# Kernel optimization log

Hardware: AMD Instinct MI355X
Metric: run time of the kernel (lower is better)

## Reference

```python
import jax, jax.numpy as jnp
import numpy as np

B, NN, F, C, L = 64, 1024, 128, 128, 4   # graphs, nodes/graph, in_feat, hidden=out, GIN layers
N = B * NN                                # total nodes = 65536
E = 1_048_576                             # total edges (avg degree 16)
SLOPE = 0.01

def leaky(x):
    return jnp.where(x >= 0, x, SLOPE * x)

def setup_inputs() -> dict:
    key = jax.random.key(0)
    ks = jax.random.split(key, 12)
    s = 0.05
    return {
        "x": jax.random.normal(ks[0], (N, F), jnp.float32),
        "W1": jax.random.normal(ks[1], (L, F, C), jnp.float32) * s,
        "b1": jnp.zeros((L, C), jnp.float32),
        "W2": jax.random.normal(ks[2], (L, C, C), jnp.float32) * s,
        "b2": jnp.zeros((L, C), jnp.float32),
        "fc1_w": jax.random.normal(ks[3], (1, C), jnp.float32) * s,
        "fc1_b": jnp.zeros((1,), jnp.float32),
        "fc2_w": jax.random.normal(ks[4], (2, NN), jnp.float32) * s,
        "fc2_b": jnp.zeros((2,), jnp.float32),
        "edge_index": jax.random.randint(ks[5], (2, E), 0, N, dtype=jnp.int64),
        "batch": jax.random.randint(ks[6], (N,), 0, B, dtype=jnp.int64),
    }

def reference(x, W1, b1, W2, b2, fc1_w, fc1_b, fc2_w, fc2_b, edge_index, batch):
    src, dst = edge_index[0], edge_index[1]
    h = x
    for l in range(L):
        # GINConv: (1+eps)*x + sum_{j->i} x_j, eps=0; then MLP Lin->LeakyReLU->Lin
        agg = jax.ops.segment_sum(h[src], dst, num_segments=N)   # [N, C]
        h = h + agg
        h = leaky(h @ W1[l] + b1[l]) @ W2[l] + b2[l]
        if l < L - 1:                                            # BasicGNN act after all but last conv
            h = leaky(h)
    h = h.reshape(B, NN, C)
    y = (leaky(h) @ fc1_w.T + fc1_b).reshape(B, NN)              # FC1: C -> 1
    logits = leaky(y) @ fc2_w.T + fc2_b                         # FC2: NN -> 2
    return jax.nn.log_softmax(logits, axis=1)
```

## Files before the change

### kernel.cpp

```cpp
#include <hip/hip_runtime.h>
#include <hip/hip_bf16.h>

#define NTOT   65536
#define CDIM   128
#define NE     1048576
#define NGRAPH 64
#define NNODE  1024
#define NLAYER 4
#define SLOPE  0.01f
#define PAD    64

typedef __attribute__((ext_vector_type(8))) short short8;
typedef __attribute__((ext_vector_type(4))) float f32x4;
typedef __attribute__((ext_vector_type(8))) unsigned short ushort8v;
typedef unsigned int u32;
typedef unsigned short u16;

__device__ __forceinline__ float bf2f_lo(u32 v){ return __uint_as_float(v << 16); }
__device__ __forceinline__ float bf2f_hi(u32 v){ return __uint_as_float(v & 0xffff0000u); }
__device__ __forceinline__ u16 f2bf(float f){
    u32 u = __float_as_uint(f);
    u += 0x7fffu + ((u >> 16) & 1u);
    return (u16)(u >> 16);
}
__device__ __forceinline__ float lk(float x){ return x >= 0.f ? x : SLOPE * x; }

__device__ __forceinline__ void accm(float* a, uint4 w, bool pr){
    float f = pr ? 1.f : 0.f;
    a[0] = fmaf(f, bf2f_lo(w.x), a[0]); a[1] = fmaf(f, bf2f_hi(w.x), a[1]);
    a[2] = fmaf(f, bf2f_lo(w.y), a[2]); a[3] = fmaf(f, bf2f_hi(w.y), a[3]);
    a[4] = fmaf(f, bf2f_lo(w.z), a[4]); a[5] = fmaf(f, bf2f_hi(w.z), a[5]);
    a[6] = fmaf(f, bf2f_lo(w.w), a[6]); a[7] = fmaf(f, bf2f_hi(w.w), a[7]);
}

__global__ void k_cast_x(const float* __restrict__ x, u16* __restrict__ h){
    int i = blockIdx.x * 256 + threadIdx.x;
    const float4* x4 = (const float4*)x;
    float4 a = x4[i * 2], b = x4[i * 2 + 1];
    u32 r0 = (u32)f2bf(a.x) | ((u32)f2bf(a.y) << 16);
    u32 r1 = (u32)f2bf(a.z) | ((u32)f2bf(a.w) << 16);
    u32 r2 = (u32)f2bf(b.x) | ((u32)f2bf(b.y) << 16);
    u32 r3 = (u32)f2bf(b.z) | ((u32)f2bf(b.w) << 16);
    ((uint4*)h)[i] = make_uint4(r0, r1, r2, r3);
}

__global__ void k_conv_w(const float* __restrict__ W1, const float* __restrict__ W2,
                         u16* __restrict__ Wt){
    int idx = blockIdx.x * 256 + threadIdx.x;
    int k = idx & 127;
    int c = (idx >> 7) & 127;
    int g = (idx >> 14) & 1;
    int l = idx >> 15;
    const float* W = g ? W2 : W1;
    Wt[idx] = f2bf(W[(l * 128 + k) * 128 + c]);
}

__global__ void k_fillx(const int* __restrict__ src, const int* __restrict__ dst,
                        int* __restrict__ cnt, u16* __restrict__ csrp){
    int part = blockIdx.x & 7;
    int g    = blockIdx.x >> 3;
    int e0   = g * 2048 + threadIdx.x * 8;
    int4 d0 = *(const int4*)(dst + e0);
    int4 d1 = *(const int4*)(dst + e0 + 4);
    int4 s0 = *(const int4*)(src + e0);
    int4 s1 = *(const int4*)(src + e0 + 4);
    int d, s, p;
    #define DO_EDGE(dd, ss) d = (dd); s = (ss); \
        if ((d >> 13) == part){ p = atomicAdd(&cnt[d], 1); if (p < PAD) csrp[d * PAD + p] = (u16)s; }
    DO_EDGE(d0.x, s0.x); DO_EDGE(d0.y, s0.y); DO_EDGE(d0.z, s0.z); DO_EDGE(d0.w, s0.w);
    DO_EDGE(d1.x, s1.x); DO_EDGE(d1.y, s1.y); DO_EDGE(d1.z, s1.z); DO_EDGE(d1.w, s1.w);
    #undef DO_EDGE
}

#define LD8(P, I) \
    P##0 = h4[(size_t)(I)[0] * 16 + l16c]; \
    P##1 = h4[(size_t)(I)[1] * 16 + l16c]; \
    P##2 = h4[(size_t)(I)[2] * 16 + l16c]; \
    P##3 = h4[(size_t)(I)[3] * 16 + l16c]; \
    P##4 = h4[(size_t)(I)[4] * 16 + l16c]; \
    P##5 = h4[(size_t)(I)[5] * 16 + l16c]; \
    P##6 = h4[(size_t)(I)[6] * 16 + l16c]; \
    P##7 = h4[(size_t)(I)[7] * 16 + l16c];

#define ACC8P(P, base) \
    accm(a0, P##0, (base) + 0 < e); accm(a1, P##1, (base) + 1 < e); \
    accm(a0, P##2, (base) + 2 < e); accm(a1, P##3, (base) + 3 < e); \
    accm(a0, P##4, (base) + 4 < e); accm(a1, P##5, (base) + 5 < e); \
    accm(a0, P##6, (base) + 6 < e); accm(a1, P##7, (base) + 7 < e);

__global__ __launch_bounds__(256) void k_layer16(const u16* __restrict__ h,
                                                 const int* __restrict__ cnt,
                                                 const u16* __restrict__ csrp,
                                                 const u16* __restrict__ Wt,
                                                 const float* __restrict__ b1,
                                                 const float* __restrict__ b2,
                                                 u16* __restrict__ hout,
                                                 const float* __restrict__ fc1_w,
                                                 const float* __restrict__ fc1_b,
                                                 float* __restrict__ y,
                                                 int layer, int act, int fuse_fc1){
    __shared__ __align__(16) u16 t_lds[16][136];
    __shared__ __align__(16) u16 u_lds[16][136];
    __shared__ float fcp[4][16];
    int tid = threadIdx.x;
    int nb  = blockIdx.x;

    {
        int row  = tid >> 4;
        int l16c = tid & 15;
        int n = nb * 16 + row;
        const uint4* h4 = (const uint4*)h;
        int e = min(cnt[n], PAD);
        const u16* rowp = csrp + (size_t)n * PAD;
        int nch = (e + 7) >> 3;

        float a0[8], a1[8];
        uint4 v = h4[(size_t)n * 16 + l16c];
        a0[0] = bf2f_lo(v.x); a0[1] = bf2f_hi(v.x);
        a0[2] = bf2f_lo(v.y); a0[3] = bf2f_hi(v.y);
        a0[4] = bf2f_lo(v.z); a0[5] = bf2f_hi(v.z);
        a0[6] = bf2f_lo(v.w); a0[7] = bf2f_hi(v.w);
        for (int f = 0; f < 8; ++f) a1[f] = 0.f;

        uint4 A0, A1, A2, A3, A4, A5, A6, A7;
        uint4 B0, B1, B2, B3, B4, B5, B6, B7;
        ushort8v zer = (ushort8v)0;

        ushort8v iA = *(const ushort8v*)(rowp);
        if (nch < 1) iA = zer;
        LD8(A, iA);
        ushort8v iB = *(const ushort8v*)(rowp + 8);

        int c = 0;
        while (c < nch){
            ushort8v iu = (c + 1 < nch) ? iB : zer;
            LD8(B, iu);
            iA = *(const ushort8v*)(rowp + (size_t)(c + 2) * 8);
            ACC8P(A, c * 8);
            ++c;
            if (c >= nch) break;
            ushort8v iv = (c + 1 < nch) ? iA : zer;
            LD8(A, iv);
            iB = *(const ushort8v*)(rowp + (size_t)(c + 2) * 8);
            ACC8P(B, c * 8);
            ++c;
        }

        u32 r0 = (u32)f2bf(a0[0] + a1[0]) | ((u32)f2bf(a0[1] + a1[1]) << 16);
        u32 r1 = (u32)f2bf(a0[2] + a1[2]) | ((u32)f2bf(a0[3] + a1[3]) << 16);
        u32 r2 = (u32)f2bf(a0[4] + a1[4]) | ((u32)f2bf(a0[5] + a1[5]) << 16);
        u32 r3 = (u32)f2bf(a0[6] + a1[6]) | ((u32)f2bf(a0[7] + a1[7]) << 16);
        *(uint4*)(&t_lds[row][l16c * 8]) = make_uint4(r0, r1, r2, r3);
    }
    __syncthreads();

    int wid = tid >> 6, lane = tid & 63;
    int l16 = lane & 15, kg = lane >> 4;
    const u16* Wt1 = Wt + (size_t)(layer * 2) * 16384;
    const u16* Wt2 = Wt1 + 16384;

    f32x4 acc[2];
    acc[0] = (f32x4){0.f, 0.f, 0.f, 0.f};
    acc[1] = (f32x4){0.f, 0.f, 0.f, 0.f};
    for (int ks = 0; ks < 4; ++ks){
        int k0 = ks * 32 + kg * 8;
        short8 afrag = *(const short8*)(&t_lds[l16][k0]);
        for (int f = 0; f < 2; ++f){
            short8 bfrag = *(const short8*)(Wt1 + (size_t)(wid * 32 + f * 16 + l16) * 128 + k0);
            acc[f] = __builtin_amdgcn_mfma_f32_16x16x32_bf16(afrag, bfrag, acc[f], 0, 0, 0);
        }
    }
    for (int f = 0; f < 2; ++f){
        int col = wid * 32 + f * 16 + l16;
        float bv = b1[layer * 128 + col];
        for (int j = 0; j < 4; ++j)
            u_lds[kg * 4 + j][col] = f2bf(lk(acc[f][j] + bv));
    }
    __syncthreads();

    f32x4 acc2[2];
    acc2[0] = (f32x4){0.f, 0.f, 0.f, 0.f};
    acc2[1] = (f32x4){0.f, 0.f, 0.f, 0.f};
    for (int ks = 0; ks < 4; ++ks){
        int k0 = ks * 32 + kg * 8;
        short8 afrag = *(const short8*)(&u_lds[l16][k0]);
        for (int f = 0; f < 2; ++f){
            short8 bfrag = *(const short8*)(Wt2 + (size_t)(wid * 32 + f * 16 + l16) * 128 + k0);
            acc2[f] = __builtin_amdgcn_mfma_f32_16x16x32_bf16(afrag, bfrag, acc2[f], 0, 0, 0);
        }
    }

    if (fuse_fc1){
        float part[4] = {0.f, 0.f, 0.f, 0.f};
        for (int f = 0; f < 2; ++f){
            int col = wid * 32 + f * 16 + l16;
            float bv = b2[layer * 128 + col];
            float wv = fc1_w[col];
            for (int j = 0; j < 4; ++j)
                part[j] += lk(acc2[f][j] + bv) * wv;
        }
        for (int off = 8; off; off >>= 1)
            for (int j = 0; j < 4; ++j)
                part[j] += __shfl_xor(part[j], off, 64);
        if (l16 == 0)
            for (int j = 0; j < 4; ++j)
                fcp[wid][kg * 4 + j] = part[j];
        __syncthreads();
        if (tid < 16)
            y[nb * 16 + tid] = fcp[0][tid] + fcp[1][tid] + fcp[2][tid] + fcp[3][tid] + fc1_b[0];
    } else {
        for (int f = 0; f < 2; ++f){
            int col = wid * 32 + f * 16 + l16;
            float bv = b2[layer * 128 + col];
            for (int j = 0; j < 4; ++j){
                float v = acc2[f][j] + bv;
                if (act) v = lk(v);
                hout[(size_t)(nb * 16 + kg * 4 + j) * 128 + col] = f2bf(v);
            }
        }
    }
}

__global__ void k_fc2(const float* __restrict__ y, const float* __restrict__ fc2_w,
                      const float* __restrict__ fc2_b, float* __restrict__ out){
    int b = blockIdx.x, tid = threadIdx.x;
    float a0 = 0.f, a1 = 0.f;
    for (int j = tid; j < 1024; j += 256){
        float v = lk(y[b * 1024 + j]);
        a0 += v * fc2_w[j];
        a1 += v * fc2_w[1024 + j];
    }
    for (int off = 32; off; off >>= 1){
        a0 += __shfl_xor(a0, off, 64);
        a1 += __shfl_xor(a1, off, 64);
    }
    __shared__ float s0[4], s1[4];
    int wid = tid >> 6, lane = tid & 63;
    if (lane == 0){ s0[wid] = a0; s1[wid] = a1; }
    __syncthreads();
    if (tid == 0){
        float l0 = s0[0] + s0[1] + s0[2] + s0[3] + fc2_b[0];
        float l1 = s1[0] + s1[1] + s1[2] + s1[3] + fc2_b[1];
        float m = fmaxf(l0, l1);
        float lse = m + logf(expf(l0 - m) + expf(l1 - m));
        out[b * 2 + 0] = l0 - lse;
        out[b * 2 + 1] = l1 - lse;
    }
}

extern "C" void kernel_launch(void* const* d_in, const int* in_sizes, int n_in,
                              void* d_out, int out_size, void* d_ws, size_t ws_size,
                              hipStream_t stream){
    (void)in_sizes; (void)n_in; (void)out_size; (void)ws_size;
    const float* x     = (const float*)d_in[0];
    const float* W1    = (const float*)d_in[1];
    const float* b1    = (const float*)d_in[2];
    const float* W2    = (const float*)d_in[3];
    const float* b2    = (const float*)d_in[4];
    const float* fc1_w = (const float*)d_in[5];
    const float* fc1_b = (const float*)d_in[6];
    const float* fc2_w = (const float*)d_in[7];
    const float* fc2_b = (const float*)d_in[8];
    const int*   edges = (const int*)d_in[9];
    const int*   esrc  = edges;
    const int*   edst  = edges + NE;

    char* w = (char*)d_ws;
    u16* ha  = (u16*)w;           w += (size_t)NTOT * CDIM * 2;
    u16* hb  = (u16*)w;           w += (size_t)NTOT * CDIM * 2;
    u16* Wt  = (u16*)w;           w += (size_t)NLAYER * 2 * CDIM * CDIM * 2;
    float* y = (float*)w;         w += (size_t)NTOT * 4;
    int* cnt = (int*)w;           w += (size_t)NTOT * 4;
    u16* csrp = (u16*)w;          w += (size_t)(NTOT + 2) * PAD * 2;

    hipMemsetAsync(cnt, 0, (size_t)NTOT * 4, stream);
    k_cast_x<<<4096, 256, 0, stream>>>(x, ha);
    k_conv_w<<<512, 256, 0, stream>>>(W1, W2, Wt);
    k_fillx <<<4096, 256, 0, stream>>>(esrc, edst, cnt, csrp);

    u16* hin = ha;
    u16* hout = hb;
    for (int l = 0; l < NLAYER; ++l){
        k_layer16<<<4096, 256, 0, stream>>>(hin, cnt, csrp, Wt, b1, b2, hout,
                                            fc1_w, fc1_b, y,
                                            l, (l < NLAYER - 1) ? 1 : 0,
                                            (l == NLAYER - 1) ? 1 : 0);
        u16* tmp = hin; hin = hout; hout = tmp;
    }
    k_fc2<<<NGRAPH, 256, 0, stream>>>(y, fc2_w, fc2_b, (float*)d_out);
}
```

Baseline: 306.8 us.

## Split each node's edge gather across two half-warps with 512-thread blocks

Doubles the block to 512 threads so each node's neighbour list is split between two 16-lane groups that gather alternate 8-edge chunks, then combined with a cross-lane shuffle. The MFMA stage is reshaped so each of the 8 waves owns 16 output columns instead of 32, and the fc1 reduction sums 8 wave partials. The aim is to raise memory-level parallelism in the latency-bound gather and halve per-thread serial chain length. The cost is more threads per block, extra shuffles, and the CSR padding is enlarged to cover the deeper prefetch reads.

```diff
diff --git a/kernel.cpp b/kernel.cpp
--- a/kernel.cpp
+++ b/kernel.cpp
@@ -88,7 +88,7 @@
     accm(a0, P##4, (base) + 4 < e); accm(a1, P##5, (base) + 5 < e); \
     accm(a0, P##6, (base) + 6 < e); accm(a1, P##7, (base) + 7 < e);
 
-__global__ __launch_bounds__(256) void k_layer16(const u16* __restrict__ h,
+__global__ __launch_bounds__(512) void k_layer16(const u16* __restrict__ h,
                                                  const int* __restrict__ cnt,
                                                  const u16* __restrict__ csrp,
                                                  const u16* __restrict__ Wt,
@@ -101,26 +101,25 @@
                                                  int layer, int act, int fuse_fc1){
     __shared__ __align__(16) u16 t_lds[16][136];
     __shared__ __align__(16) u16 u_lds[16][136];
-    __shared__ float fcp[4][16];
+    __shared__ float fcp[8][16];
     int tid = threadIdx.x;
     int nb  = blockIdx.x;
 
     {
-        int row  = tid >> 4;
-        int l16c = tid & 15;
-        int n = nb * 16 + row;
+        int nodei = tid >> 5;
+        int sub   = tid & 31;
+        int l16c  = sub & 15;
+        int eg    = sub >> 4;
+        int n = nb * 16 + nodei;
         const uint4* h4 = (const uint4*)h;
         int e = min(cnt[n], PAD);
-        const u16* rowp = csrp + (size_t)n * PAD;
-        int nch = (e + 7) >> 3;
+        const u16* rowp = csrp + (size_t)n * PAD + eg * 8;
+        int nch = (e + 15) >> 4;
 
         float a0[8], a1[8];
+        for (int f = 0; f < 8; ++f){ a0[f] = 0.f; a1[f] = 0.f; }
         uint4 v = h4[(size_t)n * 16 + l16c];
-        a0[0] = bf2f_lo(v.x); a0[1] = bf2f_hi(v.x);
-        a0[2] = bf2f_lo(v.y); a0[3] = bf2f_hi(v.y);
-        a0[4] = bf2f_lo(v.z); a0[5] = bf2f_hi(v.z);
-        a0[6] = bf2f_lo(v.w); a0[7] = bf2f_hi(v.w);
-        for (int f = 0; f < 8; ++f) a1[f] = 0.f;
+        accm(a0, v, eg == 0);
 
         uint4 A0, A1, A2, A3, A4, A5, A6, A7;
         uint4 B0, B1, B2, B3, B4, B5, B6, B7;
@@ -129,28 +128,39 @@
         ushort8v iA = *(const ushort8v*)(rowp);
         if (nch < 1) iA = zer;
         LD8(A, iA);
-        ushort8v iB = *(const ushort8v*)(rowp + 8);
+        ushort8v iB = *(const ushort8v*)(rowp + 16);
 
         int c = 0;
         while (c < nch){
             ushort8v iu = (c + 1 < nch) ? iB : zer;
             LD8(B, iu);
-            iA = *(const ushort8v*)(rowp + (size_t)(c + 2) * 8);
-            ACC8P(A, c * 8);
+            iA = *(const ushort8v*)(rowp + (size_t)(c + 2) * 16);
+            ACC8P(A, c * 16 + eg * 8);
             ++c;
             if (c >= nch) break;
             ushort8v iv = (c + 1 < nch) ? iA : zer;
             LD8(A, iv);
-            iB = *(const ushort8v*)(rowp + (size_t)(c + 2) * 8);
-            ACC8P(B, c * 8);
+            iB = *(const ushort8v*)(rowp + (size_t)(c + 2) * 16);
+            ACC8P(B, c * 16 + eg * 8);
             ++c;
         }
 
-        u32 r0 = (u32)f2bf(a0[0] + a1[0]) | ((u32)f2bf(a0[1] + a1[1]) << 16);
-        u32 r1 = (u32)f2bf(a0[2] + a1[2]) | ((u32)f2bf(a0[3] + a1[3]) << 16);
-        u32 r2 = (u32)f2bf(a0[4] + a1[4]) | ((u32)f2bf(a0[5] + a1[5]) << 16);
-        u32 r3 = (u32)f2bf(a0[6] + a1[6]) | ((u32)f2bf(a0[7] + a1[7]) << 16);
-        *(uint4*)(&t_lds[row][l16c * 8]) = make_uint4(r0, r1, r2, r3);
+        float s0 = a0[0] + a1[0], s1 = a0[1] + a1[1];
+        float s2 = a0[2] + a1[2], s3 = a0[3] + a1[3];
+        float s4 = a0[4] + a1[4], s5 = a0[5] + a1[5];
+        float s6 = a0[6] + a1[6], s7 = a0[7] + a1[7];
+        s0 += __shfl_xor(s0, 16, 64); s1 += __shfl_xor(s1, 16, 64);
+        s2 += __shfl_xor(s2, 16, 64); s3 += __shfl_xor(s3, 16, 64);
+        s4 += __shfl_xor(s4, 16, 64); s5 += __shfl_xor(s5, 16, 64);
+        s6 += __shfl_xor(s6, 16, 64); s7 += __shfl_xor(s7, 16, 64);
+
+        if (eg == 0){
+            u32 r0 = (u32)f2bf(s0) | ((u32)f2bf(s1) << 16);
+            u32 r1 = (u32)f2bf(s2) | ((u32)f2bf(s3) << 16);
+            u32 r2 = (u32)f2bf(s4) | ((u32)f2bf(s5) << 16);
+            u32 r3 = (u32)f2bf(s6) | ((u32)f2bf(s7) << 16);
+            *(uint4*)(&t_lds[nodei][l16c * 8]) = make_uint4(r0, r1, r2, r3);
+        }
     }
     __syncthreads();
 
@@ -159,46 +169,36 @@
     const u16* Wt1 = Wt + (size_t)(layer * 2) * 16384;
     const u16* Wt2 = Wt1 + 16384;
 
-    f32x4 acc[2];
-    acc[0] = (f32x4){0.f, 0.f, 0.f, 0.f};
-    acc[1] = (f32x4){0.f, 0.f, 0.f, 0.f};
+    f32x4 acc = (f32x4){0.f, 0.f, 0.f, 0.f};
     for (int ks = 0; ks < 4; ++ks){
         int k0 = ks * 32 + kg * 8;
         short8 afrag = *(const short8*)(&t_lds[l16][k0]);
-        for (int f = 0; f < 2; ++f){
-            short8 bfrag = *(const short8*)(Wt1 + (size_t)(wid * 32 + f * 16 + l16) * 128 + k0);
-            acc[f] = __builtin_amdgcn_mfma_f32_16x16x32_bf16(afrag, bfrag, acc[f], 0, 0, 0);
-        }
-    }
-    for (int f = 0; f < 2; ++f){
-        int col = wid * 32 + f * 16 + l16;
+        short8 bfrag = *(const short8*)(Wt1 + (size_t)(wid * 16 + l16) * 128 + k0);
+        acc = __builtin_amdgcn_mfma_f32_16x16x32_bf16(afrag, bfrag, acc, 0, 0, 0);
+    }
+    {
+        int col = wid * 16 + l16;
         float bv = b1[layer * 128 + col];
         for (int j = 0; j < 4; ++j)
-            u_lds[kg * 4 + j][col] = f2bf(lk(acc[f][j] + bv));
+            u_lds[kg * 4 + j][col] = f2bf(lk(acc[j] + bv));
     }
     __syncthreads();
 
-    f32x4 acc2[2];
-    acc2[0] = (f32x4){0.f, 0.f, 0.f, 0.f};
-    acc2[1] = (f32x4){0.f, 0.f, 0.f, 0.f};
+    f32x4 acc2 = (f32x4){0.f, 0.f, 0.f, 0.f};
     for (int ks = 0; ks < 4; ++ks){
         int k0 = ks * 32 + kg * 8;
         short8 afrag = *(const short8*)(&u_lds[l16][k0]);
-        for (int f = 0; f < 2; ++f){
-            short8 bfrag = *(const short8*)(Wt2 + (size_t)(wid * 32 + f * 16 + l16) * 128 + k0);
-            acc2[f] = __builtin_amdgcn_mfma_f32_16x16x32_bf16(afrag, bfrag, acc2[f], 0, 0, 0);
-        }
+        short8 bfrag = *(const short8*)(Wt2 + (size_t)(wid * 16 + l16) * 128 + k0);
+        acc2 = __builtin_amdgcn_mfma_f32_16x16x32_bf16(afrag, bfrag, acc2, 0, 0, 0);
     }
 
     if (fuse_fc1){
-        float part[4] = {0.f, 0.f, 0.f, 0.f};
-        for (int f = 0; f < 2; ++f){
-            int col = wid * 32 + f * 16 + l16;
-            float bv = b2[layer * 128 + col];
-            float wv = fc1_w[col];
-            for (int j = 0; j < 4; ++j)
-                part[j] += lk(acc2[f][j] + bv) * wv;
-        }
+        int col = wid * 16 + l16;
+        float bv = b2[layer * 128 + col];
+        float wv = fc1_w[col];
+        float part[4];
+        for (int j = 0; j < 4; ++j)
+            part[j] = lk(acc2[j] + bv) * wv;
         for (int off = 8; off; off >>= 1)
             for (int j = 0; j < 4; ++j)
                 part[j] += __shfl_xor(part[j], off, 64);
@@ -206,17 +206,18 @@
             for (int j = 0; j < 4; ++j)
                 fcp[wid][kg * 4 + j] = part[j];
         __syncthreads();
-        if (tid < 16)
-            y[nb * 16 + tid] = fcp[0][tid] + fcp[1][tid] + fcp[2][tid] + fcp[3][tid] + fc1_b[0];
+        if (tid < 16){
+            float s = fc1_b[0];
+            for (int w8 = 0; w8 < 8; ++w8) s += fcp[w8][tid];
+            y[nb * 16 + tid] = s;
+        }
     } else {
-        for (int f = 0; f < 2; ++f){
-            int col = wid * 32 + f * 16 + l16;
-            float bv = b2[layer * 128 + col];
-            for (int j = 0; j < 4; ++j){
-                float v = acc2[f][j] + bv;
-                if (act) v = lk(v);
-                hout[(size_t)(nb * 16 + kg * 4 + j) * 128 + col] = f2bf(v);
-            }
+        int col = wid * 16 + l16;
+        float bv = b2[layer * 128 + col];
+        for (int j = 0; j < 4; ++j){
+            float v = acc2[j] + bv;
+            if (act) v = lk(v);
+            hout[(size_t)(nb * 16 + kg * 4 + j) * 128 + col] = f2bf(v);
         }
     }
 }
@@ -271,7 +272,7 @@
     u16* Wt  = (u16*)w;           w += (size_t)NLAYER * 2 * CDIM * CDIM * 2;
     float* y = (float*)w;         w += (size_t)NTOT * 4;
     int* cnt = (int*)w;           w += (size_t)NTOT * 4;
-    u16* csrp = (u16*)w;          w += (size_t)(NTOT + 2) * PAD * 2;
+    u16* csrp = (u16*)w;          w += (size_t)(NTOT + 4) * PAD * 2;
 
     hipMemsetAsync(cnt, 0, (size_t)NTOT * 4, stream);
     k_cast_x<<<4096, 256, 0, stream>>>(x, ha);
@@ -281,7 +282,7 @@
     u16* hin = ha;
     u16* hout = hb;
     for (int l = 0; l < NLAYER; ++l){
-        k_layer16<<<4096, 256, 0, stream>>>(hin, cnt, csrp, Wt, b1, b2, hout,
+        k_layer16<<<4096, 512, 0, stream>>>(hin, cnt, csrp, Wt, b1, b2, hout,
                                             fc1_w, fc1_b, y,
                                             l, (l < NLAYER - 1) ? 1 : 0,
                                             (l == NLAYER - 1) ? 1 : 0);
```

After: 340.5 us. +11.0%, slower.
